# Performance work log

Measured on AMD Instinct MI355X. Metric: run time of the kernel, lower is better.

## Reference

```python
import jax, jax.numpy as jnp
import numpy as np

N_NODES = 131072
N_EDGES = 4194304
H1, H2 = 16, 1


def setup_inputs() -> dict:
    key = jax.random.key(0)
    k = jax.random.split(key, 6)
    x = jax.random.uniform(k[0], (N_NODES, 2), dtype=jnp.float32)
    edge_index = jax.random.randint(k[1], (2, N_EDGES), 0, N_NODES, dtype=jnp.int64)
    # GCNConv weights (glorot-ish scale) and zero biases
    W1 = jax.random.normal(k[2], (2, H1), dtype=jnp.float32) * 0.5
    b1 = jnp.zeros((H1,), dtype=jnp.float32)
    W2 = jax.random.normal(k[3], (H1, H2), dtype=jnp.float32) * 0.25
    b2 = jnp.zeros((H2,), dtype=jnp.float32)
    return {"x": x, "W1": W1, "b1": b1, "W2": W2, "b2": b2, "edge_index": edge_index}


def gcn_layer(x, W, b, src, dst, n):
    # PyG GCNConv: h = D^{-1/2} (A+I) D^{-1/2} (x W) + b  (self-loops already in src/dst)
    h = x @ W                                              # [N, F_out]
    deg = jax.ops.segment_sum(jnp.ones(dst.shape[0], h.dtype), dst, num_segments=n)
    dinv = jax.lax.rsqrt(deg)                              # deg >= 1 thanks to self-loops
    norm = dinv[src] * dinv[dst]                           # [E+N]
    out = jax.ops.segment_sum(h[src] * norm[:, None], dst, num_segments=n)
    return out + b


def reference(x, W1, b1, W2, b2, edge_index):
    n = x.shape[0]
    loops = jnp.arange(n, dtype=edge_index.dtype)
    src = jnp.concatenate([edge_index[0], loops])          # add self-loops once
    dst = jnp.concatenate([edge_index[1], loops])
    h = jax.nn.relu(gcn_layer(x, W1, b1, src, dst, n))
    h = gcn_layer(h, W2, b2, src, dst, n)                  # [N, 1]
    scores = jax.nn.sigmoid(h)
    return scores[edge_index[0]]                           # gather per-edge source score [E, 1]
```

## Files before the change

kernel.cpp:

```cpp
#include <hip/hip_runtime.h>
#include <cmath>

typedef unsigned int uint;
typedef unsigned long long ull;

constexpr int N  = 131072;
constexpr int E  = 4194304;
constexpr int F  = 16;
constexpr int NB = 512;
constexpr int NBLK  = 512;
constexpr int SCT   = 512;
constexpr int GT    = 1024;
constexpr int CHUNK = 8192;
constexpr int EPT   = 16;
constexpr int CAPB  = 9216;
constexpr int LT    = 1024;
constexpr uint SENT = 0xFFFFFFFFu;

constexpr float S1 = 4194304.0f;
constexpr float S2 = 65536.0f;
constexpr int  BIAS = 1 << 22;

__global__ void __launch_bounds__(SCT) k_scatter(
        const int* __restrict__ src, const int* __restrict__ dst,
        uint* __restrict__ part, uint* __restrict__ dirw) {
    __shared__ uint h[NB];
    __shared__ uint wsum[8];
    __shared__ uint vals[CHUNK];
    int t = threadIdx.x, g = blockIdx.x;
    int lane = t & 63, w = t >> 6;
    h[t] = 0;
    __syncthreads();
    int d[EPT], s[EPT];
    const int4* src4 = (const int4*)src;
    const int4* dst4 = (const int4*)dst;
    int base4 = g * (CHUNK / 4);
#pragma unroll
    for (int k = 0; k < EPT / 4; ++k) {
        int4 d4 = dst4[base4 + k * SCT + t];
        int4 s4 = src4[base4 + k * SCT + t];
        d[4 * k + 0] = d4.x; d[4 * k + 1] = d4.y; d[4 * k + 2] = d4.z; d[4 * k + 3] = d4.w;
        s[4 * k + 0] = s4.x; s[4 * k + 1] = s4.y; s[4 * k + 2] = s4.z; s[4 * k + 3] = s4.w;
        atomicAdd(&h[d4.x >> 8], 1u);
        atomicAdd(&h[d4.y >> 8], 1u);
        atomicAdd(&h[d4.z >> 8], 1u);
        atomicAdd(&h[d4.w >> 8], 1u);
    }
    __syncthreads();
    uint v = h[t];
    uint sv = v;
#pragma unroll
    for (int off = 1; off < 64; off <<= 1) {
        uint n = __shfl_up(sv, off);
        if (lane >= off) sv += n;
    }
    if (lane == 63) wsum[w] = sv;
    __syncthreads();
    uint wo = 0;
    for (int i = 0; i < w; ++i) wo += wsum[i];
    sv += wo;
    uint ex = sv - v;
    dirw[(size_t)g * NB + t] = v | (ex << 16);
    __syncthreads();
    h[t] = ex;
    __syncthreads();
#pragma unroll
    for (int k = 0; k < EPT; ++k) {
        int b = d[k] >> 8;
        uint slot = atomicAdd(&h[b], 1u);
        vals[slot] = ((uint)s[k] << 8) | (uint)(d[k] & 255);
    }
    __syncthreads();
    uint4* part4 = (uint4*)(part + (size_t)g * CHUNK);
    const uint4* vals4 = (const uint4*)vals;
#pragma unroll
    for (int k = 0; k < EPT / 4; ++k)
        part4[k * SCT + t] = vals4[k * SCT + t];
}

__global__ void __launch_bounds__(GT) k_gather(
        const uint* __restrict__ part, const uint* __restrict__ dirw,
        const float* __restrict__ x,
        uint* __restrict__ part2, uint* __restrict__ blen,
        uint* __restrict__ degg,
        float* __restrict__ dinv, float2* __restrict__ y) {
    __shared__ uint ps[NB + 1];
    __shared__ uint segoff[NB];
    __shared__ uint hw[16 * 256];
    __shared__ uint wsum[8];
    int t = threadIdx.x, b = blockIdx.x;
    int lane = t & 63, w = t >> 6;
#pragma unroll
    for (int k = 0; k < 4; ++k) hw[k * GT + t] = 0;
    if (t < NB) {
        uint pd = dirw[(size_t)t * NB + b];
        uint len = pd & 0xFFFFu;
        segoff[t] = (uint)t * CHUNK + (pd >> 16);
        uint sv = len;
#pragma unroll
        for (int off = 1; off < 64; off <<= 1) {
            uint n = __shfl_up(sv, off);
            if (lane >= off) sv += n;
        }
        if (lane == 63) wsum[w] = sv;
        ps[t] = sv - len;
    }
    __syncthreads();
    if (t < NB) {
        uint wo = 0;
        for (int i = 0; i < w; ++i) wo += wsum[i];
        ps[t] += wo;
    }
    if (t == 0) {
        uint Lt = 0;
#pragma unroll
        for (int i = 0; i < 8; ++i) Lt += wsum[i];
        ps[NB] = Lt;
    }
    __syncthreads();
    uint L = ps[NB];
    uint* o2 = part2 + (size_t)b * CAPB;
    int sub = lane >> 4, l16 = lane & 15;
#pragma unroll
    for (int pass = 0; pass < 8; ++pass) {
        int r = pass * 64 + w * 4 + sub;
        uint off = segoff[r], base = ps[r], len = ps[r + 1] - base;
        for (uint j = l16; j < len; j += 16) {
            uint pk = part[off + j];
            atomicAdd(&hw[w * 256 + (pk & 255u)], 1u);
            if (base + j < (uint)CAPB) o2[base + j] = pk;
        }
    }
    __syncthreads();
    uint Lc = (L > (uint)CAPB) ? (uint)CAPB : L;
    uint Lp = (Lc + 3u) & ~3u;
    uint i2 = Lc + (uint)t;
    if (i2 < Lp) o2[i2] = SENT;
    if (t == 0) blen[b] = Lp;
    if (t < 256) {
        uint c = 0;
#pragma unroll
        for (int k = 0; k < 16; ++k) c += hw[k * 256 + t];
        int node = (b << 8) + t;
        degg[node] = c;
        float di = rsqrtf(1.0f + (float)c);
        dinv[node] = di;
        float2 xv = ((const float2*)x)[node];
        y[node] = make_float2(di * xv.x, di * xv.y);
    }
}

__global__ void __launch_bounds__(LT) k_l1(
        const uint* __restrict__ part2, const uint* __restrict__ blen,
        const float2* __restrict__ y, const float* __restrict__ dinv,
        const uint* __restrict__ degg,
        const float* __restrict__ W1, const float* __restrict__ b1,
        const float* __restrict__ W2, float* __restrict__ g2) {
    __shared__ ull aa[16 * 256];
    int t = threadIdx.x, b = blockIdx.x, w = t >> 6;
#pragma unroll
    for (int k = 0; k < 4; ++k) aa[k * LT + t] = 0ull;
    __syncthreads();
    uint L4 = blen[b] >> 2;
    const uint4* p4 = (const uint4*)(part2 + (size_t)b * CAPB);
    uint i = t;
    uint4 q = (i < L4) ? p4[i] : make_uint4(SENT, SENT, SENT, SENT);
    while (i < L4) {
        uint in = i + LT;
        uint4 qn = (in < L4) ? p4[in] : make_uint4(SENT, SENT, SENT, SENT);
        bool v0 = q.x != SENT, v1 = q.y != SENT, v2 = q.z != SENT, v3 = q.w != SENT;
        float2 y0, y1, y2, y3;
        if (v0) y0 = y[q.x >> 8];
        if (v1) y1 = y[q.y >> 8];
        if (v2) y2 = y[q.z >> 8];
        if (v3) y3 = y[q.w >> 8];
        if (v0) {
            uint i0 = (uint)(__float2int_rn(y0.x * S1) + BIAS);
            uint i1 = (uint)(__float2int_rn(y0.y * S1) + BIAS);
            atomicAdd(&aa[w * 256 + (q.x & 255u)], (ull)i0 | ((ull)i1 << 32));
        }
        if (v1) {
            uint i0 = (uint)(__float2int_rn(y1.x * S1) + BIAS);
            uint i1 = (uint)(__float2int_rn(y1.y * S1) + BIAS);
            atomicAdd(&aa[w * 256 + (q.y & 255u)], (ull)i0 | ((ull)i1 << 32));
        }
        if (v2) {
            uint i0 = (uint)(__float2int_rn(y2.x * S1) + BIAS);
            uint i1 = (uint)(__float2int_rn(y2.y * S1) + BIAS);
            atomicAdd(&aa[w * 256 + (q.z & 255u)], (ull)i0 | ((ull)i1 << 32));
        }
        if (v3) {
            uint i0 = (uint)(__float2int_rn(y3.x * S1) + BIAS);
            uint i1 = (uint)(__float2int_rn(y3.y * S1) + BIAS);
            atomicAdd(&aa[w * 256 + (q.w & 255u)], (ull)i0 | ((ull)i1 << 32));
        }
        q = qn; i = in;
    }
    __syncthreads();
    if (t < 256) {
        uint s0b = 0, s1b = 0;
#pragma unroll
        for (int k = 0; k < 16; ++k) {
            ull v = aa[k * 256 + t];
            s0b += (uint)v;
            s1b += (uint)(v >> 32);
        }
        int node = (b << 8) + t;
        uint deg = degg[node];
        int s0 = (int)(s0b - deg * (uint)BIAS);
        int s1 = (int)(s1b - deg * (uint)BIAS);
        float di = dinv[node];
        float2 yn = y[node];
        float A0 = di * ((float)s0 * (1.0f / S1) + yn.x);
        float A1 = di * ((float)s1 * (1.0f / S1) + yn.y);
        float acc = 0.0f;
#pragma unroll
        for (int f = 0; f < F; ++f) {
            float v = fmaf(A0, W1[f], fmaf(A1, W1[F + f], b1[f]));
            acc = fmaf(fmaxf(v, 0.0f), W2[f], acc);
        }
        g2[node] = di * acc;
    }
}

__global__ void __launch_bounds__(LT) k_l2(
        const uint* __restrict__ part2, const uint* __restrict__ blen,
        const float* __restrict__ g2, const float* __restrict__ dinv,
        const float* __restrict__ b2, float* __restrict__ scores) {
    __shared__ int a[16 * 256];
    int t = threadIdx.x, b = blockIdx.x, w = t >> 6;
#pragma unroll
    for (int k = 0; k < 4; ++k) a[k * LT + t] = 0;
    __syncthreads();
    uint L4 = blen[b] >> 2;
    const uint4* p4 = (const uint4*)(part2 + (size_t)b * CAPB);
    uint i = t;
    uint4 q = (i < L4) ? p4[i] : make_uint4(SENT, SENT, SENT, SENT);
    while (i < L4) {
        uint in = i + LT;
        uint4 qn = (in < L4) ? p4[in] : make_uint4(SENT, SENT, SENT, SENT);
        bool v0 = q.x != SENT, v1 = q.y != SENT, v2 = q.z != SENT, v3 = q.w != SENT;
        float f0, f1, f2, f3;
        if (v0) f0 = g2[q.x >> 8];
        if (v1) f1 = g2[q.y >> 8];
        if (v2) f2 = g2[q.z >> 8];
        if (v3) f3 = g2[q.w >> 8];
        if (v0) atomicAdd(&a[w * 256 + (q.x & 255u)], __float2int_rn(f0 * S2));
        if (v1) atomicAdd(&a[w * 256 + (q.y & 255u)], __float2int_rn(f1 * S2));
        if (v2) atomicAdd(&a[w * 256 + (q.z & 255u)], __float2int_rn(f2 * S2));
        if (v3) atomicAdd(&a[w * 256 + (q.w & 255u)], __float2int_rn(f3 * S2));
        q = qn; i = in;
    }
    __syncthreads();
    if (t < 256) {
        int s = 0;
#pragma unroll
        for (int k = 0; k < 16; ++k) s += a[k * 256 + t];
        int node = (b << 8) + t;
        float acc = (float)s * (1.0f / S2);
        float v = fmaf(dinv[node], acc + g2[node], b2[0]);
        scores[node] = 1.0f / (1.0f + expf(-v));
    }
}

__global__ void k_out(const int* __restrict__ src, const float* __restrict__ scores,
                      float* __restrict__ out) {
    int i = blockIdx.x * blockDim.x + threadIdx.x;
    if (i >= E / 8) return;
    const int4* s4p = (const int4*)src;
    int4 sa = s4p[2 * i], sb = s4p[2 * i + 1];
    float4 oa, ob;
    oa.x = scores[sa.x];
    oa.y = scores[sa.y];
    oa.z = scores[sa.z];
    oa.w = scores[sa.w];
    ob.x = scores[sb.x];
    ob.y = scores[sb.y];
    ob.z = scores[sb.z];
    ob.w = scores[sb.w];
    ((float4*)out)[2 * i]     = oa;
    ((float4*)out)[2 * i + 1] = ob;
}

extern "C" void kernel_launch(void* const* d_in, const int* in_sizes, int n_in,
                              void* d_out, int out_size, void* d_ws, size_t ws_size,
                              hipStream_t stream) {
    const float* x  = (const float*)d_in[0];
    const float* W1 = (const float*)d_in[1];
    const float* b1 = (const float*)d_in[2];
    const float* W2 = (const float*)d_in[3];
    const float* b2 = (const float*)d_in[4];
    const int*   ei = (const int*)d_in[5];
    const int* src = ei;
    const int* dst = ei + E;

    uint*   dirw   = (uint*)d_ws;
    uint*   blen   = dirw + (size_t)NB * NB;
    uint*   degg   = blen + NB;
    float*  dinv   = (float*)(degg + N);
    float2* y      = (float2*)(dinv + N);
    float*  g2     = (float*)(y + N);
    float*  scores = g2 + N;
    uint*   part2  = (uint*)(scores + N);

    uint* part  = (uint*)d_out;
    float* out  = (float*)d_out;

    k_scatter<<<NBLK,        SCT, 0, stream>>>(src, dst, part, dirw);
    k_gather <<<NB,          GT,  0, stream>>>(part, dirw, x, part2, blen, degg,
                                               dinv, y);
    k_l1     <<<NB,          LT,  0, stream>>>(part2, blen, y, dinv, degg,
                                               W1, b1, W2, g2);
    k_l2     <<<NB,          LT,  0, stream>>>(part2, blen, g2, dinv, b2, scores);
    k_out    <<<E / 8 / 256, 256, 0, stream>>>(src, scores, out);
}
```

Before: 166.4 us.

## Build per-node CSR in gather and replace atomic aggregation with segmented reductions

The gather kernel now stages each bucket's edges in shared memory, prefix-sums per-node degrees and counting-sorts edges into destination-node order. Each node gets a start offset, which yields a CSR layout. The two layer kernels then use 16-lane groups per node that sum neighbour features with shuffles, replacing the fixed-point LDS atomics. This removes the quantisation and atomic contention and gives exact float sums, but it adds a second pass with shared-memory atomics in gather, and load balance now depends on node degree.

```diff
diff --git a/kernel.cpp b/kernel.cpp
--- a/kernel.cpp
+++ b/kernel.cpp
@@ -2,7 +2,6 @@
 #include <cmath>
 
 typedef unsigned int uint;
-typedef unsigned long long ull;
 
 constexpr int N  = 131072;
 constexpr int E  = 4194304;
@@ -15,11 +14,6 @@
 constexpr int EPT   = 16;
 constexpr int CAPB  = 9216;
 constexpr int LT    = 1024;
-constexpr uint SENT = 0xFFFFFFFFu;
-
-constexpr float S1 = 4194304.0f;
-constexpr float S2 = 65536.0f;
-constexpr int  BIAS = 1 << 22;
 
 __global__ void __launch_bounds__(SCT) k_scatter(
         const int* __restrict__ src, const int* __restrict__ dst,
@@ -81,12 +75,12 @@
 __global__ void __launch_bounds__(GT) k_gather(
         const uint* __restrict__ part, const uint* __restrict__ dirw,
         const float* __restrict__ x,
-        uint* __restrict__ part2, uint* __restrict__ blen,
-        uint* __restrict__ degg,
-        float* __restrict__ dinv, float2* __restrict__ y) {
+        uint* __restrict__ part2, uint* __restrict__ nstart,
+        uint* __restrict__ degg, float* __restrict__ dinv, float2* __restrict__ y) {
     __shared__ uint ps[NB + 1];
     __shared__ uint segoff[NB];
     __shared__ uint hw[16 * 256];
+    __shared__ uint stage[CAPB];
     __shared__ uint wsum[8];
     int t = threadIdx.x, b = blockIdx.x;
     int lane = t & 63, w = t >> 6;
@@ -118,8 +112,6 @@
         ps[NB] = Lt;
     }
     __syncthreads();
-    uint L = ps[NB];
-    uint* o2 = part2 + (size_t)b * CAPB;
     int sub = lane >> 4, l16 = lane & 15;
 #pragma unroll
     for (int pass = 0; pass < 8; ++pass) {
@@ -128,138 +120,120 @@
         for (uint j = l16; j < len; j += 16) {
             uint pk = part[off + j];
             atomicAdd(&hw[w * 256 + (pk & 255u)], 1u);
-            if (base + j < (uint)CAPB) o2[base + j] = pk;
-        }
-    }
-    __syncthreads();
-    uint Lc = (L > (uint)CAPB) ? (uint)CAPB : L;
-    uint Lp = (Lc + 3u) & ~3u;
-    uint i2 = Lc + (uint)t;
-    if (i2 < Lp) o2[i2] = SENT;
-    if (t == 0) blen[b] = Lp;
+            if (base + j < (uint)CAPB) stage[base + j] = pk;
+        }
+    }
+    __syncthreads();
+    uint degc = 0, svn = 0;
     if (t < 256) {
         uint c = 0;
 #pragma unroll
-        for (int k = 0; k < 16; ++k) c += hw[k * 256 + t];
+        for (int k = 0; k < 16; ++k) {
+            uint v0 = hw[k * 256 + t];
+            hw[k * 256 + t] = c;
+            c += v0;
+        }
+        degc = c;
+        svn = c;
+#pragma unroll
+        for (int off = 1; off < 64; off <<= 1) {
+            uint n2 = __shfl_up(svn, off);
+            if (lane >= off) svn += n2;
+        }
+        if (lane == 63) wsum[w] = svn;
+    }
+    __syncthreads();
+    if (t < 256) {
+        uint wo = 0;
+        for (int i = 0; i < w; ++i) wo += wsum[i];
+        uint ex = svn - degc + wo;
+#pragma unroll
+        for (int k = 0; k < 16; ++k) hw[k * 256 + t] += ex;
         int node = (b << 8) + t;
-        degg[node] = c;
-        float di = rsqrtf(1.0f + (float)c);
+        nstart[node] = ex;
+        degg[node]   = degc;
+        float di = rsqrtf(1.0f + (float)degc);
         dinv[node] = di;
         float2 xv = ((const float2*)x)[node];
         y[node] = make_float2(di * xv.x, di * xv.y);
     }
+    __syncthreads();
+    uint* o2 = part2 + (size_t)b * CAPB;
+#pragma unroll
+    for (int pass = 0; pass < 8; ++pass) {
+        int r = pass * 64 + w * 4 + sub;
+        uint base = ps[r], len = ps[r + 1] - base;
+        for (uint j = l16; j < len; j += 16) {
+            if (base + j < (uint)CAPB) {
+                uint pk = stage[base + j];
+                uint pos = atomicAdd(&hw[w * 256 + (pk & 255u)], 1u);
+                if (pos < (uint)CAPB) o2[pos] = pk >> 8;
+            }
+        }
+    }
 }
 
 __global__ void __launch_bounds__(LT) k_l1(
-        const uint* __restrict__ part2, const uint* __restrict__ blen,
+        const uint* __restrict__ part2, const uint* __restrict__ nstart,
+        const uint* __restrict__ degg,
         const float2* __restrict__ y, const float* __restrict__ dinv,
-        const uint* __restrict__ degg,
         const float* __restrict__ W1, const float* __restrict__ b1,
         const float* __restrict__ W2, float* __restrict__ g2) {
-    __shared__ ull aa[16 * 256];
-    int t = threadIdx.x, b = blockIdx.x, w = t >> 6;
-#pragma unroll
-    for (int k = 0; k < 4; ++k) aa[k * LT + t] = 0ull;
-    __syncthreads();
-    uint L4 = blen[b] >> 2;
-    const uint4* p4 = (const uint4*)(part2 + (size_t)b * CAPB);
-    uint i = t;
-    uint4 q = (i < L4) ? p4[i] : make_uint4(SENT, SENT, SENT, SENT);
-    while (i < L4) {
-        uint in = i + LT;
-        uint4 qn = (in < L4) ? p4[in] : make_uint4(SENT, SENT, SENT, SENT);
-        bool v0 = q.x != SENT, v1 = q.y != SENT, v2 = q.z != SENT, v3 = q.w != SENT;
-        float2 y0, y1, y2, y3;
-        if (v0) y0 = y[q.x >> 8];
-        if (v1) y1 = y[q.y >> 8];
-        if (v2) y2 = y[q.z >> 8];
-        if (v3) y3 = y[q.w >> 8];
-        if (v0) {
-            uint i0 = (uint)(__float2int_rn(y0.x * S1) + BIAS);
-            uint i1 = (uint)(__float2int_rn(y0.y * S1) + BIAS);
-            atomicAdd(&aa[w * 256 + (q.x & 255u)], (ull)i0 | ((ull)i1 << 32));
-        }
-        if (v1) {
-            uint i0 = (uint)(__float2int_rn(y1.x * S1) + BIAS);
-            uint i1 = (uint)(__float2int_rn(y1.y * S1) + BIAS);
-            atomicAdd(&aa[w * 256 + (q.y & 255u)], (ull)i0 | ((ull)i1 << 32));
-        }
-        if (v2) {
-            uint i0 = (uint)(__float2int_rn(y2.x * S1) + BIAS);
-            uint i1 = (uint)(__float2int_rn(y2.y * S1) + BIAS);
-            atomicAdd(&aa[w * 256 + (q.z & 255u)], (ull)i0 | ((ull)i1 << 32));
-        }
-        if (v3) {
-            uint i0 = (uint)(__float2int_rn(y3.x * S1) + BIAS);
-            uint i1 = (uint)(__float2int_rn(y3.y * S1) + BIAS);
-            atomicAdd(&aa[w * 256 + (q.w & 255u)], (ull)i0 | ((ull)i1 << 32));
-        }
-        q = qn; i = in;
-    }
-    __syncthreads();
-    if (t < 256) {
-        uint s0b = 0, s1b = 0;
-#pragma unroll
-        for (int k = 0; k < 16; ++k) {
-            ull v = aa[k * 256 + t];
-            s0b += (uint)v;
-            s1b += (uint)(v >> 32);
-        }
-        int node = (b << 8) + t;
-        uint deg = degg[node];
-        int s0 = (int)(s0b - deg * (uint)BIAS);
-        int s1 = (int)(s1b - deg * (uint)BIAS);
+    int t = threadIdx.x, b = blockIdx.x;
+    int grp = t >> 4, l16 = t & 15;
+    float w1a = W1[l16], w1b = W1[F + l16], bb = b1[l16], w2 = W2[l16];
+    const uint* p2 = part2 + (size_t)b * CAPB;
+#pragma unroll
+    for (int idx = 0; idx < 4; ++idx) {
+        int n = idx * 64 + grp;
+        int node = (b << 8) + n;
+        uint s = nstart[node], d = degg[node];
+        float a0 = 0.0f, a1 = 0.0f;
+        for (uint j = l16; j < d; j += 16) {
+            float2 yv = y[p2[s + j]];
+            a0 += yv.x; a1 += yv.y;
+        }
+#pragma unroll
+        for (int off = 8; off >= 1; off >>= 1) {
+            a0 += __shfl_down(a0, off, 16);
+            a1 += __shfl_down(a1, off, 16);
+        }
+        a0 = __shfl(a0, 0, 16);
+        a1 = __shfl(a1, 0, 16);
         float di = dinv[node];
         float2 yn = y[node];
-        float A0 = di * ((float)s0 * (1.0f / S1) + yn.x);
-        float A1 = di * ((float)s1 * (1.0f / S1) + yn.y);
-        float acc = 0.0f;
-#pragma unroll
-        for (int f = 0; f < F; ++f) {
-            float v = fmaf(A0, W1[f], fmaf(A1, W1[F + f], b1[f]));
-            acc = fmaf(fmaxf(v, 0.0f), W2[f], acc);
-        }
-        g2[node] = di * acc;
+        float A0 = di * (a0 + yn.x);
+        float A1 = di * (a1 + yn.y);
+        float v = fmaf(A0, w1a, fmaf(A1, w1b, bb));
+        float r = fmaxf(v, 0.0f) * w2;
+#pragma unroll
+        for (int off = 8; off >= 1; off >>= 1) r += __shfl_down(r, off, 16);
+        if (l16 == 0) g2[node] = di * r;
     }
 }
 
 __global__ void __launch_bounds__(LT) k_l2(
-        const uint* __restrict__ part2, const uint* __restrict__ blen,
+        const uint* __restrict__ part2, const uint* __restrict__ nstart,
+        const uint* __restrict__ degg,
         const float* __restrict__ g2, const float* __restrict__ dinv,
         const float* __restrict__ b2, float* __restrict__ scores) {
-    __shared__ int a[16 * 256];
-    int t = threadIdx.x, b = blockIdx.x, w = t >> 6;
-#pragma unroll
-    for (int k = 0; k < 4; ++k) a[k * LT + t] = 0;
-    __syncthreads();
-    uint L4 = blen[b] >> 2;
-    const uint4* p4 = (const uint4*)(part2 + (size_t)b * CAPB);
-    uint i = t;
-    uint4 q = (i < L4) ? p4[i] : make_uint4(SENT, SENT, SENT, SENT);
-    while (i < L4) {
-        uint in = i + LT;
-        uint4 qn = (in < L4) ? p4[in] : make_uint4(SENT, SENT, SENT, SENT);
-        bool v0 = q.x != SENT, v1 = q.y != SENT, v2 = q.z != SENT, v3 = q.w != SENT;
-        float f0, f1, f2, f3;
-        if (v0) f0 = g2[q.x >> 8];
-        if (v1) f1 = g2[q.y >> 8];
-        if (v2) f2 = g2[q.z >> 8];
-        if (v3) f3 = g2[q.w >> 8];
-        if (v0) atomicAdd(&a[w * 256 + (q.x & 255u)], __float2int_rn(f0 * S2));
-        if (v1) atomicAdd(&a[w * 256 + (q.y & 255u)], __float2int_rn(f1 * S2));
-        if (v2) atomicAdd(&a[w * 256 + (q.z & 255u)], __float2int_rn(f2 * S2));
-        if (v3) atomicAdd(&a[w * 256 + (q.w & 255u)], __float2int_rn(f3 * S2));
-        q = qn; i = in;
-    }
-    __syncthreads();
-    if (t < 256) {
-        int s = 0;
-#pragma unroll
-        for (int k = 0; k < 16; ++k) s += a[k * 256 + t];
-        int node = (b << 8) + t;
-        float acc = (float)s * (1.0f / S2);
-        float v = fmaf(dinv[node], acc + g2[node], b2[0]);
-        scores[node] = 1.0f / (1.0f + expf(-v));
+    int t = threadIdx.x, b = blockIdx.x;
+    int grp = t >> 4, l16 = t & 15;
+    float bb = b2[0];
+    const uint* p2 = part2 + (size_t)b * CAPB;
+#pragma unroll
+    for (int idx = 0; idx < 4; ++idx) {
+        int n = idx * 64 + grp;
+        int node = (b << 8) + n;
+        uint s = nstart[node], d = degg[node];
+        float a = 0.0f;
+        for (uint j = l16; j < d; j += 16) a += g2[p2[s + j]];
+#pragma unroll
+        for (int off = 8; off >= 1; off >>= 1) a += __shfl_down(a, off, 16);
+        if (l16 == 0) {
+            float v = fmaf(dinv[node], a + g2[node], bb);
+            scores[node] = 1.0f / (1.0f + expf(-v));
+        }
     }
 }
 
@@ -295,8 +269,8 @@
     const int* dst = ei + E;
 
     uint*   dirw   = (uint*)d_ws;
-    uint*   blen   = dirw + (size_t)NB * NB;
-    uint*   degg   = blen + NB;
+    uint*   nstart = dirw + (size_t)NB * NB;
+    uint*   degg   = nstart + N;
     float*  dinv   = (float*)(degg + N);
     float2* y      = (float2*)(dinv + N);
     float*  g2     = (float*)(y + N);
@@ -307,10 +281,11 @@
     float* out  = (float*)d_out;
 
     k_scatter<<<NBLK,        SCT, 0, stream>>>(src, dst, part, dirw);
-    k_gather <<<NB,          GT,  0, stream>>>(part, dirw, x, part2, blen, degg,
-                                               dinv, y);
-    k_l1     <<<NB,          LT,  0, stream>>>(part2, blen, y, dinv, degg,
+    k_gather <<<NB,          GT,  0, stream>>>(part, dirw, x, part2, nstart,
+                                               degg, dinv, y);
+    k_l1     <<<NB,          LT,  0, stream>>>(part2, nstart, degg, y, dinv,
                                                W1, b1, W2, g2);
-    k_l2     <<<NB,          LT,  0, stream>>>(part2, blen, g2, dinv, b2, scores);
+    k_l2     <<<NB,          LT,  0, stream>>>(part2, nstart, degg, g2, dinv,
+                                               b2, scores);
     k_out    <<<E / 8 / 256, 256, 0, stream>>>(src, scores, out);
 }
```

Result: slower. 186.1 us (+11.9%).
